# Kernel optimization log

Hardware: AMD Instinct MI355X
Metric: run time of the kernel (lower is better)

Reference implementation:

```python
import jax, jax.numpy as jnp
import numpy as np

EPS = 1e-8


def setup_inputs() -> dict:
    key = jax.random.key(0)
    k1, k2, k3, k4 = jax.random.split(key, 4)
    N, E, d = 10000, 5000, 128
    F = jax.random.normal(k1, (N, d), dtype=jnp.float32)
    H = jax.random.uniform(k2, (N, E), dtype=jnp.float32)
    Dv = jax.random.uniform(k3, (N, N), dtype=jnp.float32)
    De = jax.random.uniform(k4, (E, E), dtype=jnp.float32)
    return {"F": F, "H": H, "Dv": Dv, "De": De}


def reference(F, H, Dv, De):
    # Only the diagonals of Dv/De are used by the original (torch.diag extraction).
    dv = jnp.diagonal(Dv)                      # [N]
    de = jnp.diagonal(De)                      # [E]
    dv_inv_sqrt = (dv + EPS) ** -0.5           # diag of Dv^{-1/2}
    de_inv = 1.0 / (de + EPS)                  # diag of De^{-1}
    # L = I - Dv^{-1/2} H De^{-1} H^T Dv^{-1/2}
    # trace(F^T L F) = ||F||_F^2 - sum_e de_inv[e] * ||(H^T (Dv^{-1/2} F))[e]||^2
    Fs = F * dv_inv_sqrt[:, None]              # [N, d]
    M = H.T @ Fs                               # [E, d]
    trace_term = jnp.sum(F * F) - jnp.sum(de_inv[:, None] * (M * M))
    # use_rayleigh=False; reduction='mean' -> divide by N
    loss = trace_term / F.shape[0]
    return loss
```

## Files before the change

kernel.cpp:

```cpp
#include <hip/hip_runtime.h>

#define EPSF 1e-8f

typedef __attribute__((ext_vector_type(8))) short bf16x8;
typedef __attribute__((ext_vector_type(4))) float f32x4;

constexpr int Nv     = 10000;
constexpr int Ne     = 5000;
constexpr int Dd     = 128;
constexpr int NPAD   = 10016;
constexpr int EPAD   = 5120;
constexpr int KSTEPS = 313;
constexpr int KSPLIT = 16;
constexpr int STEPS_PER = (KSTEPS + KSPLIT - 1) / KSPLIT;

__device__ __forceinline__ unsigned short f2bf_rne(float f) {
    unsigned int u = __builtin_bit_cast(unsigned int, f);
    u += 0x7fffu + ((u >> 16) & 1u);
    return (unsigned short)(u >> 16);
}

__global__ void prep_de_kernel(const float* __restrict__ De, float* __restrict__ de_inv) {
    int e = blockIdx.x * 256 + threadIdx.x;
    if (e < EPAD) de_inv[e] = (e < Ne) ? 1.0f / (De[(size_t)e * (Ne + 1)] + EPSF) : 0.0f;
}

__global__ void prep_fst_kernel(const float* __restrict__ F, const float* __restrict__ Dv,
                                short* __restrict__ Fst) {
    int n = blockIdx.x * 256 + threadIdx.x;
    int c = blockIdx.y;
    if (n < NPAD) {
        unsigned short b = 0;
        if (n < Nv) {
            float s = 1.0f / sqrtf(Dv[(size_t)n * (Nv + 1)] + EPSF);
            b = f2bf_rne(F[(size_t)n * Dd + c] * s);
        }
        Fst[(size_t)c * NPAD + n] = (short)b;
    }
}

__global__ void sum_ff_kernel(const float* __restrict__ F, float* __restrict__ out0) {
    const float4* F4 = (const float4*)F;
    int base = blockIdx.x * 512 + threadIdx.x;
    float4 a = F4[base];
    float4 b = F4[base + 256];
    float sum = a.x*a.x + a.y*a.y + a.z*a.z + a.w*a.w
              + b.x*b.x + b.y*b.y + b.z*b.z + b.w*b.w;
    #pragma unroll
    for (int off = 32; off; off >>= 1) sum += __shfl_down(sum, off);
    if ((threadIdx.x & 63) == 0) atomicAdd(out0, sum);
}

__global__ __launch_bounds__(256, 2)
void gemm_split_kernel(const float* __restrict__ H, const short* __restrict__ Fst,
                       float* __restrict__ M) {
    __shared__ unsigned int Alds[128 * 20];

    const int t  = threadIdx.x;
    const int w  = t >> 6;
    const int l  = t & 63;
    const int lm = l & 15;
    const int q  = l >> 4;
    const int e0 = blockIdx.x * 128;
    const int sb = blockIdx.y * STEPS_PER;
    const int se = min(sb + STEPS_PER, KSTEPS);

    const int rp  = t & 15;
    const int cp4 = t >> 4;

    f32x4 acc[2][8];
    #pragma unroll
    for (int a = 0; a < 2; ++a)
        #pragma unroll
        for (int b = 0; b < 8; ++b) acc[a][b] = (f32x4){0.f, 0.f, 0.f, 0.f};

    for (int s = sb; s < se; ++s) {
        const int n0 = s * 32;

        bf16x8 Bf[8];
        #pragma unroll
        for (int cb = 0; cb < 8; ++cb) {
            const int c = cb * 16 + lm;
            Bf[cb] = *(const bf16x8*)(Fst + (size_t)c * NPAD + n0 + q * 8);
        }

        const int n  = n0 + 2 * rp;
        const bool vn = (n < Nv);
        #pragma unroll
        for (int j = 0; j < 4; ++j) {
            const int cp = cp4 + 16 * j;
            const int el = 2 * cp;
            const int e  = e0 + el;
            float2 a0 = make_float2(0.f, 0.f), a1 = make_float2(0.f, 0.f);
            if (vn && e < Ne) {
                a0 = *(const float2*)(H + (size_t)n * Ne + e);
                a1 = *(const float2*)(H + (size_t)(n + 1) * Ne + e);
            }
            unsigned int w0 = (unsigned int)f2bf_rne(a0.x) | ((unsigned int)f2bf_rne(a1.x) << 16);
            unsigned int w1 = (unsigned int)f2bf_rne(a0.y) | ((unsigned int)f2bf_rne(a1.y) << 16);
            Alds[el * 20 + rp]       = w0;
            Alds[(el + 1) * 20 + rp] = w1;
        }
        __syncthreads();

        bf16x8 Af[2];
        #pragma unroll
        for (int eb = 0; eb < 2; ++eb) {
            const int el = (2 * w + eb) * 16 + lm;
            Af[eb] = *(const bf16x8*)((const char*)Alds + el * 80 + q * 16);
        }
        __syncthreads();

        #pragma unroll
        for (int cb = 0; cb < 8; ++cb)
            #pragma unroll
            for (int eb = 0; eb < 2; ++eb)
                acc[eb][cb] = __builtin_amdgcn_mfma_f32_16x16x32_bf16(
                    Af[eb], Bf[cb], acc[eb][cb], 0, 0, 0);
    }

    #pragma unroll
    for (int eb = 0; eb < 2; ++eb) {
        #pragma unroll
        for (int cb = 0; cb < 8; ++cb) {
            const int c = cb * 16 + lm;
            #pragma unroll
            for (int r = 0; r < 4; ++r) {
                const int el = (2 * w + eb) * 16 + q * 4 + r;
                atomicAdd(&M[(size_t)(e0 + el) * 128 + c], acc[eb][cb][r]);
            }
        }
    }
}

__global__ void reduce_m_kernel(const float* __restrict__ M, const float* __restrict__ de_inv,
                                float* __restrict__ outS) {
    const float4* M4 = (const float4*)M;
    int base = blockIdx.x * 512 + threadIdx.x;
    float sum = 0.f;
    #pragma unroll
    for (int i = 0; i < 2; ++i) {
        int idx = base + i * 256;
        float4 m = M4[idx];
        float wgt = de_inv[idx >> 5];
        sum += wgt * (m.x*m.x + m.y*m.y + m.z*m.z + m.w*m.w);
    }
    #pragma unroll
    for (int off = 32; off; off >>= 1) sum += __shfl_down(sum, off);
    if ((threadIdx.x & 63) == 0) atomicAdd(outS, sum);
}

__global__ void final_kernel(const float* __restrict__ ws0, float* __restrict__ out) {
    out[0] = (ws0[0] - ws0[1]) * (1.0f / (float)Nv);
}

extern "C" void kernel_launch(void* const* d_in, const int* in_sizes, int n_in,
                              void* d_out, int out_size, void* d_ws, size_t ws_size,
                              hipStream_t stream) {
    (void)in_sizes; (void)n_in; (void)out_size; (void)ws_size;
    const float* F  = (const float*)d_in[0];
    const float* H  = (const float*)d_in[1];
    const float* Dv = (const float*)d_in[2];
    const float* De = (const float*)d_in[3];
    float* out = (float*)d_out;

    float* ws0    = (float*)d_ws;
    float* M      = ws0 + 16;
    float* de_inv = M + (size_t)EPAD * 128;
    short* Fst    = (short*)(de_inv + EPAD);

    hipMemsetAsync(d_ws, 0, 64 + (size_t)EPAD * 128 * 4, stream);

    prep_de_kernel <<<EPAD / 256, 256, 0, stream>>>(De, de_inv);
    prep_fst_kernel<<<dim3((NPAD + 255) / 256, 128), 256, 0, stream>>>(F, Dv, Fst);
    sum_ff_kernel  <<<625, 256, 0, stream>>>(F, ws0);
    gemm_split_kernel<<<dim3(EPAD / 128, KSPLIT), 256, 0, stream>>>(H, Fst, M);
    reduce_m_kernel<<<320, 256, 0, stream>>>(M, de_inv, ws0 + 1);
    final_kernel   <<<1, 1, 0, stream>>>(ws0, out);
}
```

Before: 709.5 us.

## Double-buffer H tiles, use 512-thread GEMM blocks, replace atomics with split partials

The GEMM kernel now prefetches the next H tile into registers while computing the current one. It uses double-buffered LDS with a single barrier per step, and runs 512 threads per block so each wave covers a 32x64 output tile. Split-K partial results are written to separate buffers instead of atomically added, and the reduce kernel sums them and computes de_inv inline. This removes the large M memset. The Dv diagonal is also precomputed once instead of being gathered per column, at the cost of more workspace memory and extra reads of the partials during the reduction.

```diff
diff --git a/kernel.cpp b/kernel.cpp
--- a/kernel.cpp
+++ b/kernel.cpp
@@ -11,8 +11,7 @@
 constexpr int NPAD   = 10016;
 constexpr int EPAD   = 5120;
 constexpr int KSTEPS = 313;
-constexpr int KSPLIT = 16;
-constexpr int STEPS_PER = (KSTEPS + KSPLIT - 1) / KSPLIT;
+constexpr int KSPLIT = 12;
 
 __device__ __forceinline__ unsigned short f2bf_rne(float f) {
     unsigned int u = __builtin_bit_cast(unsigned int, f);
@@ -20,21 +19,18 @@
     return (unsigned short)(u >> 16);
 }
 
-__global__ void prep_de_kernel(const float* __restrict__ De, float* __restrict__ de_inv) {
-    int e = blockIdx.x * 256 + threadIdx.x;
-    if (e < EPAD) de_inv[e] = (e < Ne) ? 1.0f / (De[(size_t)e * (Ne + 1)] + EPSF) : 0.0f;
+__global__ void prep_dv_kernel(const float* __restrict__ Dv, float* __restrict__ dvis) {
+    int n = blockIdx.x * 256 + threadIdx.x;
+    if (n < NPAD) dvis[n] = (n < Nv) ? rsqrtf(Dv[(size_t)n * (Nv + 1)] + EPSF) : 0.0f;
 }
 
-__global__ void prep_fst_kernel(const float* __restrict__ F, const float* __restrict__ Dv,
+__global__ void prep_fst_kernel(const float* __restrict__ F, const float* __restrict__ dvis,
                                 short* __restrict__ Fst) {
     int n = blockIdx.x * 256 + threadIdx.x;
     int c = blockIdx.y;
     if (n < NPAD) {
         unsigned short b = 0;
-        if (n < Nv) {
-            float s = 1.0f / sqrtf(Dv[(size_t)n * (Nv + 1)] + EPSF);
-            b = f2bf_rne(F[(size_t)n * Dd + c] * s);
-        }
+        if (n < Nv) b = f2bf_rne(F[(size_t)n * Dd + c] * dvis[n]);
         Fst[(size_t)c * NPAD + n] = (short)b;
     }
 }
@@ -51,100 +47,121 @@
     if ((threadIdx.x & 63) == 0) atomicAdd(out0, sum);
 }
 
-__global__ __launch_bounds__(256, 2)
+__global__ __launch_bounds__(512, 4)
 void gemm_split_kernel(const float* __restrict__ H, const short* __restrict__ Fst,
-                       float* __restrict__ M) {
-    __shared__ unsigned int Alds[128 * 20];
+                       float* __restrict__ Mp) {
+    __shared__ unsigned int Alds[2][128 * 20];
 
-    const int t  = threadIdx.x;
-    const int w  = t >> 6;
-    const int l  = t & 63;
-    const int lm = l & 15;
-    const int q  = l >> 4;
-    const int e0 = blockIdx.x * 128;
-    const int sb = blockIdx.y * STEPS_PER;
-    const int se = min(sb + STEPS_PER, KSTEPS);
+    const int t   = threadIdx.x;
+    const int w   = t >> 6;
+    const int l   = t & 63;
+    const int lm  = l & 15;
+    const int q   = l >> 4;
+    const int e0  = blockIdx.x * 128;
+    const int we  = (w >> 1) * 32;
+    const int wc  = (w & 1) * 64;
+    const int spl = blockIdx.y;
+    const int sb  = (spl * KSTEPS) / KSPLIT;
+    const int se  = ((spl + 1) * KSTEPS) / KSPLIT;
 
     const int rp  = t & 15;
-    const int cp4 = t >> 4;
+    const int cpb = t >> 4;
 
-    f32x4 acc[2][8];
+    float2 hcur[2][2], hnxt[2][2];
+
+    auto loadH = [&](int s, float2 (&h)[2][2]) {
+        const int n = s * 32 + 2 * rp;
+        #pragma unroll
+        for (int j = 0; j < 2; ++j) {
+            const int el = 2 * (cpb + 32 * j);
+            const int e  = e0 + el;
+            h[j][0] = make_float2(0.f, 0.f);
+            h[j][1] = make_float2(0.f, 0.f);
+            if (n < Nv && e < Ne) {
+                h[j][0] = *(const float2*)(H + (size_t)n * Ne + e);
+                h[j][1] = *(const float2*)(H + (size_t)(n + 1) * Ne + e);
+            }
+        }
+    };
+    auto writeLDS = [&](int buf, float2 (&h)[2][2]) {
+        #pragma unroll
+        for (int j = 0; j < 2; ++j) {
+            const int el = 2 * (cpb + 32 * j);
+            unsigned int w0 = (unsigned int)f2bf_rne(h[j][0].x) | ((unsigned int)f2bf_rne(h[j][1].x) << 16);
+            unsigned int w1 = (unsigned int)f2bf_rne(h[j][0].y) | ((unsigned int)f2bf_rne(h[j][1].y) << 16);
+            Alds[buf][el * 20 + rp]       = w0;
+            Alds[buf][(el + 1) * 20 + rp] = w1;
+        }
+    };
+
+    f32x4 acc[2][4];
     #pragma unroll
     for (int a = 0; a < 2; ++a)
         #pragma unroll
-        for (int b = 0; b < 8; ++b) acc[a][b] = (f32x4){0.f, 0.f, 0.f, 0.f};
+        for (int b = 0; b < 4; ++b) acc[a][b] = (f32x4){0.f, 0.f, 0.f, 0.f};
+
+    loadH(sb, hcur);
+    writeLDS(0, hcur);
+    __syncthreads();
 
     for (int s = sb; s < se; ++s) {
-        const int n0 = s * 32;
+        const int buf = (s - sb) & 1;
+        const int n0  = s * 32;
 
-        bf16x8 Bf[8];
+        if (s + 1 < se) loadH(s + 1, hnxt);
+
+        bf16x8 Bf[4];
         #pragma unroll
-        for (int cb = 0; cb < 8; ++cb) {
-            const int c = cb * 16 + lm;
+        for (int cb = 0; cb < 4; ++cb) {
+            const int c = wc + cb * 16 + lm;
             Bf[cb] = *(const bf16x8*)(Fst + (size_t)c * NPAD + n0 + q * 8);
         }
-
-        const int n  = n0 + 2 * rp;
-        const bool vn = (n < Nv);
-        #pragma unroll
-        for (int j = 0; j < 4; ++j) {
-            const int cp = cp4 + 16 * j;
-            const int el = 2 * cp;
-            const int e  = e0 + el;
-            float2 a0 = make_float2(0.f, 0.f), a1 = make_float2(0.f, 0.f);
-            if (vn && e < Ne) {
-                a0 = *(const float2*)(H + (size_t)n * Ne + e);
-                a1 = *(const float2*)(H + (size_t)(n + 1) * Ne + e);
-            }
-            unsigned int w0 = (unsigned int)f2bf_rne(a0.x) | ((unsigned int)f2bf_rne(a1.x) << 16);
-            unsigned int w1 = (unsigned int)f2bf_rne(a0.y) | ((unsigned int)f2bf_rne(a1.y) << 16);
-            Alds[el * 20 + rp]       = w0;
-            Alds[(el + 1) * 20 + rp] = w1;
-        }
-        __syncthreads();
-
         bf16x8 Af[2];
         #pragma unroll
         for (int eb = 0; eb < 2; ++eb) {
-            const int el = (2 * w + eb) * 16 + lm;
-            Af[eb] = *(const bf16x8*)((const char*)Alds + el * 80 + q * 16);
+            const int el = we + eb * 16 + lm;
+            Af[eb] = *(const bf16x8*)((const char*)Alds[buf] + el * 80 + q * 16);
         }
-        __syncthreads();
 
         #pragma unroll
-        for (int cb = 0; cb < 8; ++cb)
+        for (int cb = 0; cb < 4; ++cb)
             #pragma unroll
             for (int eb = 0; eb < 2; ++eb)
                 acc[eb][cb] = __builtin_amdgcn_mfma_f32_16x16x32_bf16(
                     Af[eb], Bf[cb], acc[eb][cb], 0, 0, 0);
+
+        if (s + 1 < se) writeLDS(buf ^ 1, hnxt);
+        __syncthreads();
     }
 
+    float* dst = Mp + (size_t)spl * EPAD * 128;
     #pragma unroll
     for (int eb = 0; eb < 2; ++eb) {
         #pragma unroll
-        for (int cb = 0; cb < 8; ++cb) {
-            const int c = cb * 16 + lm;
+        for (int cb = 0; cb < 4; ++cb) {
+            const int c = wc + cb * 16 + lm;
             #pragma unroll
             for (int r = 0; r < 4; ++r) {
-                const int el = (2 * w + eb) * 16 + q * 4 + r;
-                atomicAdd(&M[(size_t)(e0 + el) * 128 + c], acc[eb][cb][r]);
+                const int el = we + eb * 16 + q * 4 + r;
+                dst[(size_t)(e0 + el) * 128 + c] = acc[eb][cb][r];
             }
         }
     }
 }
 
-__global__ void reduce_m_kernel(const float* __restrict__ M, const float* __restrict__ de_inv,
+__global__ void reduce_m_kernel(const float* __restrict__ Mp, const float* __restrict__ De,
                                 float* __restrict__ outS) {
-    const float4* M4 = (const float4*)M;
-    int base = blockIdx.x * 512 + threadIdx.x;
-    float sum = 0.f;
+    int gid = blockIdx.x * 256 + threadIdx.x;
+    int e   = gid >> 5;
+    int c4  = (gid & 31) * 4;
+    float de_inv = (e < Ne) ? 1.0f / (De[(size_t)e * (Ne + 1)] + EPSF) : 0.0f;
+    float4 m = {0.f, 0.f, 0.f, 0.f};
     #pragma unroll
-    for (int i = 0; i < 2; ++i) {
-        int idx = base + i * 256;
-        float4 m = M4[idx];
-        float wgt = de_inv[idx >> 5];
-        sum += wgt * (m.x*m.x + m.y*m.y + m.z*m.z + m.w*m.w);
+    for (int sp = 0; sp < KSPLIT; ++sp) {
+        float4 p = *(const float4*)(Mp + (size_t)sp * EPAD * 128 + (size_t)e * 128 + c4);
+        m.x += p.x; m.y += p.y; m.z += p.z; m.w += p.w;
     }
+    float sum = de_inv * (m.x*m.x + m.y*m.y + m.z*m.z + m.w*m.w);
     #pragma unroll
     for (int off = 32; off; off >>= 1) sum += __shfl_down(sum, off);
     if ((threadIdx.x & 63) == 0) atomicAdd(outS, sum);
@@ -164,17 +181,17 @@
     const float* De = (const float*)d_in[3];
     float* out = (float*)d_out;
 
-    float* ws0    = (float*)d_ws;
-    float* M      = ws0 + 16;
-    float* de_inv = M + (size_t)EPAD * 128;
-    short* Fst    = (short*)(de_inv + EPAD);
+    float* ws0  = (float*)d_ws;
+    float* dvis = ws0 + 16;
+    float* Mp   = dvis + NPAD;
+    short* Fst  = (short*)(Mp + (size_t)KSPLIT * EPAD * 128);
 
-    hipMemsetAsync(d_ws, 0, 64 + (size_t)EPAD * 128 * 4, stream);
+    hipMemsetAsync(ws0, 0, 64, stream);
 
-    prep_de_kernel <<<EPAD / 256, 256, 0, stream>>>(De, de_inv);
-    prep_fst_kernel<<<dim3((NPAD + 255) / 256, 128), 256, 0, stream>>>(F, Dv, Fst);
+    prep_dv_kernel <<<(NPAD + 255) / 256, 256, 0, stream>>>(Dv, dvis);
+    prep_fst_kernel<<<dim3((NPAD + 255) / 256, 128), 256, 0, stream>>>(F, dvis, Fst);
     sum_ff_kernel  <<<625, 256, 0, stream>>>(F, ws0);
-    gemm_split_kernel<<<dim3(EPAD / 128, KSPLIT), 256, 0, stream>>>(H, Fst, M);
-    reduce_m_kernel<<<320, 256, 0, stream>>>(M, de_inv, ws0 + 1);
+    gemm_split_kernel<<<dim3(EPAD / 128, KSPLIT), 512, 0, stream>>>(H, Fst, Mp);
+    reduce_m_kernel<<<640, 256, 0, stream>>>(Mp, De, ws0 + 1);
     final_kernel   <<<1, 1, 0, stream>>>(ws0, out);
 }
```

Result: no change. 700.4 us (-1.3%).
